# Kernel tuning notes

Hardware: AMD Instinct MI355X
Metric: run time of the kernel (lower is better)

The kernel has to match this reference:

```python
import jax, jax.numpy as jnp
import numpy as np

D = 2          # qudit dimension
L = 22         # number of qudits; state length = D**L = 4194304
INDEX = tuple(range(L))  # rotation applied on every qudit (angle[i] indexed by qudit position)

# Generator S = Sx(j=0, k=1) on a D-level system: |0><1| + |1><0|
def _make_S():
    S = np.zeros((D, D), dtype=np.complex64)
    S[0, 1] = 1.0
    S[1, 0] = 1.0
    return jnp.asarray(S)


def setup_inputs() -> dict:
    key = jax.random.key(0)
    k1, k2, k3 = jax.random.split(key, 3)
    n = D ** L
    x_real = jax.random.normal(k1, (n,), dtype=jnp.float32)
    x_imag = jax.random.normal(k2, (n,), dtype=jnp.float32)
    angle = jax.random.uniform(k3, (L,), dtype=jnp.float32)
    return {"x_real": x_real, "x_imag": x_imag, "angle": angle}


def reference(x_real, x_imag, angle):
    # U = kron_i expm(-0.5j * angle[i] * S)  (identity on qudits not in INDEX),
    # applied as U @ x. Instead of materializing the D^L x D^L sparse unitary,
    # apply each single-qudit gate by contracting axis i of the reshaped state,
    # which is exactly the same linear map.
    S = _make_S()
    psi = (x_real + 1j * x_imag).astype(jnp.complex64).reshape((D,) * L)
    for i in range(L):
        if i in INDEX:
            M = jax.scipy.linalg.expm((-0.5j) * angle[i].astype(jnp.complex64) * S)
            # contract qudit axis i: psi'[..., a, ...] = sum_b M[a,b] psi[..., b, ...]
            psi = jnp.moveaxis(jnp.tensordot(M, psi, axes=([1], [i])), 0, i)
        # else: identity, nothing to do
    out = psi.reshape(-1)
    return jnp.stack([out.real, out.imag])  # (2, D**L) float32
```

## Files before the change

### kernel.cpp

```cpp
#include <hip/hip_runtime.h>


constexpr int NTOT = 1 << 22;

__device__ __forceinline__ void rotg(float& ar, float& ai, float& br, float& bi,
                                     float c, float s) {
    float t0 = ar, t1 = ai, t2 = br, t3 = bi;
    ar = fmaf(c, t0,  s * t3);
    ai = fmaf(c, t1, -s * t2);
    br = fmaf(c, t2,  s * t1);
    bi = fmaf(c, t3, -s * t0);
}

template<int K0, int NB, int MSH>
__device__ __forceinline__ void gatesM(float (&ar)[16], float (&ai)[16],
                                       const float* __restrict__ ang) {
    #pragma unroll
    for (int b = 0; b < NB; ++b) {
        const int m = 1 << (MSH + b);
        float c, s;
        sincosf(0.5f * ang[21 - (K0 + b)], &s, &c);
        #pragma unroll
        for (int j = 0; j < 16; ++j)
            if (!(j & m)) rotg(ar[j], ai[j], ar[j | m], ai[j | m], c, s);
    }
}

template<int XOR>
__device__ __forceinline__ void shflgate(float (&ar)[16], float (&ai)[16],
                                         float c, float s) {
    #pragma unroll
    for (int j = 0; j < 16; ++j) {
        float pr = __shfl_xor(ar[j], XOR, 64);
        float pi = __shfl_xor(ai[j], XOR, 64);
        ar[j] = fmaf(c, ar[j],  s * pi);
        ai[j] = fmaf(c, ai[j], -s * pr);
    }
}

__device__ __forceinline__ int slot(int i) { return i ^ ((i >> 4) & 15); }

__global__ __launch_bounds__(512) void rgate_A(const float* __restrict__ xr,
                                               const float* __restrict__ xi,
                                               const float* __restrict__ ang,
                                               float* __restrict__ out) {
    __shared__ float2 sv[8192];
    const int t = threadIdx.x;
    const int l = t & 63, w = t >> 6;
    const int g0 = blockIdx.x << 13;

    const int base1 = (l << 2) | ((w & 3) << 8) | ((w >> 2) << 12);

    float ar[16], ai[16];
    #pragma unroll
    for (int q = 0; q < 4; ++q) {
        const int i = base1 | (q << 10);
        float4 vr = *(const float4*)(xr + g0 + i);
        float4 vi = *(const float4*)(xi + g0 + i);
        ar[4*q+0] = vr.x; ar[4*q+1] = vr.y; ar[4*q+2] = vr.z; ar[4*q+3] = vr.w;
        ai[4*q+0] = vi.x; ai[4*q+1] = vi.y; ai[4*q+2] = vi.z; ai[4*q+3] = vi.w;
    }
    gatesM<0, 2, 0>(ar, ai, ang);
    gatesM<10, 2, 2>(ar, ai, ang);

    {
        float c, s;
        sincosf(0.5f * ang[21 - 2], &s, &c); shflgate< 1>(ar, ai, c, s);
        sincosf(0.5f * ang[21 - 3], &s, &c); shflgate< 2>(ar, ai, c, s);
        sincosf(0.5f * ang[21 - 4], &s, &c); shflgate< 4>(ar, ai, c, s);
        sincosf(0.5f * ang[21 - 5], &s, &c); shflgate< 8>(ar, ai, c, s);
        sincosf(0.5f * ang[21 - 6], &s, &c); shflgate<16>(ar, ai, c, s);
        sincosf(0.5f * ang[21 - 7], &s, &c); shflgate<32>(ar, ai, c, s);
    }

    #pragma unroll
    for (int q = 0; q < 4; ++q)
        #pragma unroll
        for (int r = 0; r < 4; ++r)
            sv[slot(base1 | (q << 10) | r)] = make_float2(ar[4*q+r], ai[4*q+r]);
    __syncthreads();

    const int base2 = ((l & 15) << 2) | (((l >> 4) & 1) << 6) | ((w & 1) << 7)
                    | ((w >> 1) << 10) | ((l >> 5) << 12);
    #pragma unroll
    for (int j = 0; j < 4; ++j)
        #pragma unroll
        for (int r = 0; r < 4; ++r) {
            float2 v = sv[slot(base2 | (j << 8) | r)];
            ar[4*j+r] = v.x; ai[4*j+r] = v.y;
        }
    gatesM<8, 2, 2>(ar, ai, ang);
    {
        float c, s;
        sincosf(0.5f * ang[21 - 12], &s, &c);
        shflgate<32>(ar, ai, c, s);
    }

    #pragma unroll
    for (int j = 0; j < 4; ++j) {
        const int i = base2 | (j << 8);
        *(float4*)(out + g0 + i)        = make_float4(ar[4*j], ar[4*j+1], ar[4*j+2], ar[4*j+3]);
        *(float4*)(out + NTOT + g0 + i) = make_float4(ai[4*j], ai[4*j+1], ai[4*j+2], ai[4*j+3]);
    }
}

__global__ __launch_bounds__(512, 4) void rgate_B(const float* __restrict__ ang,
                                                  float* __restrict__ out) {
    __shared__ float2 sv[8192];
    const int t   = threadIdx.x;
    const int bid = blockIdx.x;
    const int blk = (bid >> 3) | ((bid & 7) << 6);
    const int sub = t & 15, hw = t >> 4;
    const int lbase = (blk << 4) + sub;
    float* outr = out;
    float* outi = out + NTOT;

    float ar[16], ai[16];
    #pragma unroll
    for (int j = 0; j < 16; ++j) {
        const int g = ((j | (hw << 4)) << 13) + lbase;
        ar[j] = outr[g]; ai[j] = outi[g];
    }
    gatesM<13, 4, 0>(ar, ai, ang);

    {
        float c, s;
        sincosf(0.5f * ang[21 - 17], &s, &c);
        shflgate<16>(ar, ai, c, s);
    }

    #pragma unroll
    for (int j = 0; j < 16; ++j)
        sv[((j | (hw << 4)) << 4) + sub] = make_float2(ar[j], ai[j]);
    __syncthreads();

    #pragma unroll
    for (int j = 0; j < 16; ++j) {
        float2 v = sv[((hw | (j << 5)) << 4) + sub];
        ar[j] = v.x; ai[j] = v.y;
    }
    gatesM<18, 4, 0>(ar, ai, ang);

    #pragma unroll
    for (int j = 0; j < 16; ++j) {
        const int g = ((hw | (j << 5)) << 13) + lbase;
        outr[g] = ar[j]; outi[g] = ai[j];
    }
}

extern "C" void kernel_launch(void* const* d_in, const int* in_sizes, int n_in,
                              void* d_out, int out_size, void* d_ws, size_t ws_size,
                              hipStream_t stream) {
    const float* xr  = (const float*)d_in[0];
    const float* xi  = (const float*)d_in[1];
    const float* ang = (const float*)d_in[2];
    float* out = (float*)d_out;

    rgate_A<<<512, 512, 0, stream>>>(xr, xi, ang, out);
    rgate_B<<<512, 512, 0, stream>>>(ang, out);
}
```

Measured before the change: 109.9 us.

## Double threads per block and halve per-thread register state in both passes

Both kernels now launch 1024 threads per block, each holding 8 complex amplitudes instead of 16. The qubit-to-thread mapping is reworked so that more gates run as cross-lane shuffles and fewer as in-register rotations. The aim is to cut register pressure and raise memory-level parallelism for this bandwidth-bound pass. In exchange, rgate_A's output stores drop from float4 vectors to scalar stores and there are more shuffle steps.

```diff
diff --git a/kernel.cpp b/kernel.cpp
--- a/kernel.cpp
+++ b/kernel.cpp
@@ -12,8 +12,8 @@
     bi = fmaf(c, t3, -s * t0);
 }
 
-template<int K0, int NB, int MSH>
-__device__ __forceinline__ void gatesM(float (&ar)[16], float (&ai)[16],
+template<int K0, int NB, int MSH, int N>
+__device__ __forceinline__ void gatesM(float (&ar)[N], float (&ai)[N],
                                        const float* __restrict__ ang) {
     #pragma unroll
     for (int b = 0; b < NB; ++b) {
@@ -21,16 +21,16 @@
         float c, s;
         sincosf(0.5f * ang[21 - (K0 + b)], &s, &c);
         #pragma unroll
-        for (int j = 0; j < 16; ++j)
+        for (int j = 0; j < N; ++j)
             if (!(j & m)) rotg(ar[j], ai[j], ar[j | m], ai[j | m], c, s);
     }
 }
 
-template<int XOR>
-__device__ __forceinline__ void shflgate(float (&ar)[16], float (&ai)[16],
+template<int XOR, int N>
+__device__ __forceinline__ void shflgate(float (&ar)[N], float (&ai)[N],
                                          float c, float s) {
     #pragma unroll
-    for (int j = 0; j < 16; ++j) {
+    for (int j = 0; j < N; ++j) {
         float pr = __shfl_xor(ar[j], XOR, 64);
         float pi = __shfl_xor(ai[j], XOR, 64);
         ar[j] = fmaf(c, ar[j],  s * pi);
@@ -40,28 +40,28 @@
 
 __device__ __forceinline__ int slot(int i) { return i ^ ((i >> 4) & 15); }
 
-__global__ __launch_bounds__(512) void rgate_A(const float* __restrict__ xr,
-                                               const float* __restrict__ xi,
-                                               const float* __restrict__ ang,
-                                               float* __restrict__ out) {
+__global__ __launch_bounds__(1024) void rgate_A(const float* __restrict__ xr,
+                                                const float* __restrict__ xi,
+                                                const float* __restrict__ ang,
+                                                float* __restrict__ out) {
     __shared__ float2 sv[8192];
     const int t = threadIdx.x;
     const int l = t & 63, w = t >> 6;
     const int g0 = blockIdx.x << 13;
 
-    const int base1 = (l << 2) | ((w & 3) << 8) | ((w >> 2) << 12);
+    const int base1 = (l << 2) | (w << 8);
 
-    float ar[16], ai[16];
+    float ar[8], ai[8];
     #pragma unroll
-    for (int q = 0; q < 4; ++q) {
-        const int i = base1 | (q << 10);
+    for (int q = 0; q < 2; ++q) {
+        const int i = base1 | (q << 12);
         float4 vr = *(const float4*)(xr + g0 + i);
         float4 vi = *(const float4*)(xi + g0 + i);
         ar[4*q+0] = vr.x; ar[4*q+1] = vr.y; ar[4*q+2] = vr.z; ar[4*q+3] = vr.w;
         ai[4*q+0] = vi.x; ai[4*q+1] = vi.y; ai[4*q+2] = vi.z; ai[4*q+3] = vi.w;
     }
     gatesM<0, 2, 0>(ar, ai, ang);
-    gatesM<10, 2, 2>(ar, ai, ang);
+    gatesM<12, 1, 2>(ar, ai, ang);
 
     {
         float c, s;
@@ -74,76 +74,85 @@
     }
 
     #pragma unroll
-    for (int q = 0; q < 4; ++q)
+    for (int q = 0; q < 2; ++q)
         #pragma unroll
         for (int r = 0; r < 4; ++r)
-            sv[slot(base1 | (q << 10) | r)] = make_float2(ar[4*q+r], ai[4*q+r]);
+            sv[slot(base1 | (q << 12) | r)] = make_float2(ar[4*q+r], ai[4*q+r]);
     __syncthreads();
 
-    const int base2 = ((l & 15) << 2) | (((l >> 4) & 1) << 6) | ((w & 1) << 7)
-                    | ((w >> 1) << 10) | ((l >> 5) << 12);
+    const int base2 = (l & 31) | ((w & 7) << 5) | ((l >> 5) << 11)
+                    | ((w >> 3) << 12);
     #pragma unroll
-    for (int j = 0; j < 4; ++j)
-        #pragma unroll
-        for (int r = 0; r < 4; ++r) {
-            float2 v = sv[slot(base2 | (j << 8) | r)];
-            ar[4*j+r] = v.x; ai[4*j+r] = v.y;
-        }
-    gatesM<8, 2, 2>(ar, ai, ang);
+    for (int j = 0; j < 8; ++j) {
+        float2 v = sv[slot(base2 | (j << 8))];
+        ar[j] = v.x; ai[j] = v.y;
+    }
+    gatesM<8, 3, 0>(ar, ai, ang);
     {
         float c, s;
-        sincosf(0.5f * ang[21 - 12], &s, &c);
+        sincosf(0.5f * ang[21 - 11], &s, &c);
         shflgate<32>(ar, ai, c, s);
     }
 
     #pragma unroll
-    for (int j = 0; j < 4; ++j) {
+    for (int j = 0; j < 8; ++j) {
         const int i = base2 | (j << 8);
-        *(float4*)(out + g0 + i)        = make_float4(ar[4*j], ar[4*j+1], ar[4*j+2], ar[4*j+3]);
-        *(float4*)(out + NTOT + g0 + i) = make_float4(ai[4*j], ai[4*j+1], ai[4*j+2], ai[4*j+3]);
+        out[g0 + i]        = ar[j];
+        out[NTOT + g0 + i] = ai[j];
     }
 }
 
-__global__ __launch_bounds__(512, 4) void rgate_B(const float* __restrict__ ang,
-                                                  float* __restrict__ out) {
+__global__ __launch_bounds__(1024) void rgate_B(const float* __restrict__ ang,
+                                                float* __restrict__ out) {
     __shared__ float2 sv[8192];
     const int t   = threadIdx.x;
     const int bid = blockIdx.x;
     const int blk = (bid >> 3) | ((bid & 7) << 6);
-    const int sub = t & 15, hw = t >> 4;
+    const int sub = t & 15;
+    const int l4  = (t >> 4) & 1, l5 = (t >> 5) & 1;
+    const int w   = t >> 6;
     const int lbase = (blk << 4) + sub;
     float* outr = out;
     float* outi = out + NTOT;
 
-    float ar[16], ai[16];
+    float ar[8], ai[8];
     #pragma unroll
-    for (int j = 0; j < 16; ++j) {
-        const int g = ((j | (hw << 4)) << 13) + lbase;
+    for (int j = 0; j < 8; ++j) {
+        const int h = j | (l4 << 3) | (l5 << 4) | (w << 5);
+        const int g = (h << 13) + lbase;
         ar[j] = outr[g]; ai[j] = outi[g];
     }
-    gatesM<13, 4, 0>(ar, ai, ang);
-
+    gatesM<13, 3, 0>(ar, ai, ang);
     {
         float c, s;
-        sincosf(0.5f * ang[21 - 17], &s, &c);
-        shflgate<16>(ar, ai, c, s);
+        sincosf(0.5f * ang[21 - 16], &s, &c); shflgate<16>(ar, ai, c, s);
+        sincosf(0.5f * ang[21 - 17], &s, &c); shflgate<32>(ar, ai, c, s);
     }
 
     #pragma unroll
-    for (int j = 0; j < 16; ++j)
-        sv[((j | (hw << 4)) << 4) + sub] = make_float2(ar[j], ai[j]);
+    for (int j = 0; j < 8; ++j) {
+        const int h = j | (l4 << 3) | (l5 << 4) | (w << 5);
+        sv[(h << 4) | sub] = make_float2(ar[j], ai[j]);
+    }
     __syncthreads();
 
     #pragma unroll
-    for (int j = 0; j < 16; ++j) {
-        float2 v = sv[((hw | (j << 5)) << 4) + sub];
+    for (int j = 0; j < 8; ++j) {
+        const int h = (w & 15) | (l4 << 4) | (j << 5) | (l5 << 8);
+        float2 v = sv[(h << 4) | sub];
         ar[j] = v.x; ai[j] = v.y;
     }
-    gatesM<18, 4, 0>(ar, ai, ang);
+    gatesM<18, 3, 0>(ar, ai, ang);
+    {
+        float c, s;
+        sincosf(0.5f * ang[21 - 21], &s, &c);
+        shflgate<32>(ar, ai, c, s);
+    }
 
     #pragma unroll
-    for (int j = 0; j < 16; ++j) {
-        const int g = ((hw | (j << 5)) << 13) + lbase;
+    for (int j = 0; j < 8; ++j) {
+        const int h = (w & 15) | (l4 << 4) | (j << 5) | (l5 << 8);
+        const int g = (h << 13) + lbase;
         outr[g] = ar[j]; outi[g] = ai[j];
     }
 }
@@ -156,6 +165,6 @@
     const float* ang = (const float*)d_in[2];
     float* out = (float*)d_out;
 
-    rgate_A<<<512, 512, 0, stream>>>(xr, xi, ang, out);
-    rgate_B<<<512, 512, 0, stream>>>(ang, out);
+    rgate_A<<<512, 1024, 0, stream>>>(xr, xi, ang, out);
+    rgate_B<<<512, 1024, 0, stream>>>(ang, out);
 }
```

Measured after the change: 111.2 us. No clear change (+1.2%).

## Split first gate stage into two LDS-free kernels, making three passes total

Applied to the files above, without the earlier changes.

The first kernel, which used a shared-memory transpose, is replaced by two kernels. K1 applies the gates on the low 8 qubit bits using registers and wave shuffles. K2 then applies the gates on bits 8–12 using strided global loads. This removes the LDS round trip and the block barrier from the first stage. The cost is an extra full read and write of the 32 MB state in global memory, which is likely to outweigh the savings for a bandwidth-bound workload.

```diff
diff --git a/kernel.cpp b/kernel.cpp
--- a/kernel.cpp
+++ b/kernel.cpp
@@ -12,8 +12,8 @@
     bi = fmaf(c, t3, -s * t0);
 }
 
-template<int K0, int NB, int MSH>
-__device__ __forceinline__ void gatesM(float (&ar)[16], float (&ai)[16],
+template<int K0, int NB, int MSH, int N>
+__device__ __forceinline__ void gatesM(float (&ar)[N], float (&ai)[N],
                                        const float* __restrict__ ang) {
     #pragma unroll
     for (int b = 0; b < NB; ++b) {
@@ -21,16 +21,16 @@
         float c, s;
         sincosf(0.5f * ang[21 - (K0 + b)], &s, &c);
         #pragma unroll
-        for (int j = 0; j < 16; ++j)
+        for (int j = 0; j < N; ++j)
             if (!(j & m)) rotg(ar[j], ai[j], ar[j | m], ai[j | m], c, s);
     }
 }
 
-template<int XOR>
-__device__ __forceinline__ void shflgate(float (&ar)[16], float (&ai)[16],
+template<int XOR, int N>
+__device__ __forceinline__ void shflgate(float (&ar)[N], float (&ai)[N],
                                          float c, float s) {
     #pragma unroll
-    for (int j = 0; j < 16; ++j) {
+    for (int j = 0; j < N; ++j) {
         float pr = __shfl_xor(ar[j], XOR, 64);
         float pi = __shfl_xor(ai[j], XOR, 64);
         ar[j] = fmaf(c, ar[j],  s * pi);
@@ -38,31 +38,24 @@
     }
 }
 
-__device__ __forceinline__ int slot(int i) { return i ^ ((i >> 4) & 15); }
+__global__ __launch_bounds__(256) void rgate_K1(const float* __restrict__ xr,
+                                                const float* __restrict__ xi,
+                                                const float* __restrict__ ang,
+                                                float* __restrict__ out) {
+    const int t = threadIdx.x;
+    const int flat = (blockIdx.x << 10) | (t << 2);
 
-__global__ __launch_bounds__(512) void rgate_A(const float* __restrict__ xr,
-                                               const float* __restrict__ xi,
-                                               const float* __restrict__ ang,
-                                               float* __restrict__ out) {
-    __shared__ float2 sv[8192];
-    const int t = threadIdx.x;
-    const int l = t & 63, w = t >> 6;
-    const int g0 = blockIdx.x << 13;
-
-    const int base1 = (l << 2) | ((w & 3) << 8) | ((w >> 2) << 12);
-
-    float ar[16], ai[16];
+    float ar[8], ai[8];
     #pragma unroll
-    for (int q = 0; q < 4; ++q) {
-        const int i = base1 | (q << 10);
-        float4 vr = *(const float4*)(xr + g0 + i);
-        float4 vi = *(const float4*)(xi + g0 + i);
+    for (int q = 0; q < 2; ++q) {
+        const int i = flat | (q << 21);
+        float4 vr = *(const float4*)(xr + i);
+        float4 vi = *(const float4*)(xi + i);
         ar[4*q+0] = vr.x; ar[4*q+1] = vr.y; ar[4*q+2] = vr.z; ar[4*q+3] = vr.w;
         ai[4*q+0] = vi.x; ai[4*q+1] = vi.y; ai[4*q+2] = vi.z; ai[4*q+3] = vi.w;
     }
+
     gatesM<0, 2, 0>(ar, ai, ang);
-    gatesM<10, 2, 2>(ar, ai, ang);
-
     {
         float c, s;
         sincosf(0.5f * ang[21 - 2], &s, &c); shflgate< 1>(ar, ai, c, s);
@@ -74,22 +67,28 @@
     }
 
     #pragma unroll
-    for (int q = 0; q < 4; ++q)
-        #pragma unroll
-        for (int r = 0; r < 4; ++r)
-            sv[slot(base1 | (q << 10) | r)] = make_float2(ar[4*q+r], ai[4*q+r]);
-    __syncthreads();
+    for (int q = 0; q < 2; ++q) {
+        const int i = flat | (q << 21);
+        *(float4*)(out + i)        = make_float4(ar[4*q], ar[4*q+1], ar[4*q+2], ar[4*q+3]);
+        *(float4*)(out + NTOT + i) = make_float4(ai[4*q], ai[4*q+1], ai[4*q+2], ai[4*q+3]);
+    }
+}
 
-    const int base2 = ((l & 15) << 2) | (((l >> 4) & 1) << 6) | ((w & 1) << 7)
-                    | ((w >> 1) << 10) | ((l >> 5) << 12);
+__global__ __launch_bounds__(256) void rgate_K2(const float* __restrict__ ang,
+                                                float* __restrict__ out) {
+    const int t = threadIdx.x, b = blockIdx.x;
+    const int base = (t & 31) | (((t >> 5) & 1) << 12) | ((t >> 6) << 5)
+                   | ((b & 1) << 7) | ((b >> 1) << 13);
+    float* outr = out;
+    float* outi = out + NTOT;
+
+    float ar[16], ai[16];
     #pragma unroll
-    for (int j = 0; j < 4; ++j)
-        #pragma unroll
-        for (int r = 0; r < 4; ++r) {
-            float2 v = sv[slot(base2 | (j << 8) | r)];
-            ar[4*j+r] = v.x; ai[4*j+r] = v.y;
-        }
-    gatesM<8, 2, 2>(ar, ai, ang);
+    for (int j = 0; j < 16; ++j) ar[j] = outr[base + (j << 8)];
+    #pragma unroll
+    for (int j = 0; j < 16; ++j) ai[j] = outi[base + (j << 8)];
+
+    gatesM<8, 4, 0>(ar, ai, ang);
     {
         float c, s;
         sincosf(0.5f * ang[21 - 12], &s, &c);
@@ -97,15 +96,13 @@
     }
 
     #pragma unroll
-    for (int j = 0; j < 4; ++j) {
-        const int i = base2 | (j << 8);
-        *(float4*)(out + g0 + i)        = make_float4(ar[4*j], ar[4*j+1], ar[4*j+2], ar[4*j+3]);
-        *(float4*)(out + NTOT + g0 + i) = make_float4(ai[4*j], ai[4*j+1], ai[4*j+2], ai[4*j+3]);
-    }
+    for (int j = 0; j < 16; ++j) outr[base + (j << 8)] = ar[j];
+    #pragma unroll
+    for (int j = 0; j < 16; ++j) outi[base + (j << 8)] = ai[j];
 }
 
-__global__ __launch_bounds__(512, 4) void rgate_B(const float* __restrict__ ang,
-                                                  float* __restrict__ out) {
+__global__ __launch_bounds__(512, 4) void rgate_K3(const float* __restrict__ ang,
+                                                   float* __restrict__ out) {
     __shared__ float2 sv[8192];
     const int t   = threadIdx.x;
     const int bid = blockIdx.x;
@@ -156,6 +153,7 @@
     const float* ang = (const float*)d_in[2];
     float* out = (float*)d_out;
 
-    rgate_A<<<512, 512, 0, stream>>>(xr, xi, ang, out);
-    rgate_B<<<512, 512, 0, stream>>>(ang, out);
+    rgate_K1<<<2048, 256, 0, stream>>>(xr, xi, ang, out);
+    rgate_K2<<<1024, 256, 0, stream>>>(ang, out);
+    rgate_K3<<<512, 512, 0, stream>>>(ang, out);
 }
```

After: 115.4 us. 5.0% more time.
